# Kernel tuning notes

Measured on AMD Instinct MI355X. Metric: run time of the kernel, lower is better.

Reference implementation:

```python
import jax, jax.numpy as jnp
import numpy as np

H = 3  # hidden size (matches nn.LSTM(3, 3, ...))


def _lstm_dir(x, Wih, Whh, bih, bhh, reverse):
    """One direction of one LSTM layer. x: [B,T,D]; PyTorch gate order i,f,g,o."""
    B = x.shape[0]
    xT = jnp.swapaxes(x, 0, 1)  # [T,B,D]
    # Precompute input projection for all timesteps (memory-bound GEMM once).
    x_proj = jnp.einsum('tbd,gd->tbg', xT, Wih) + (bih + bhh)  # [T,B,4H]

    def step(carry, xp):
        h, c = carry
        gates = xp + h @ Whh.T  # [B,4H]
        i = jax.nn.sigmoid(gates[:, :H])
        f = jax.nn.sigmoid(gates[:, H:2 * H])
        g = jnp.tanh(gates[:, 2 * H:3 * H])
        o = jax.nn.sigmoid(gates[:, 3 * H:])
        c = f * c + i * g
        h = o * jnp.tanh(c)
        return (h, c), h

    init = (jnp.zeros((B, H), x.dtype), jnp.zeros((B, H), x.dtype))
    _, hs = jax.lax.scan(step, init, x_proj, reverse=reverse)
    return jnp.swapaxes(hs, 0, 1)  # [B,T,H], time-aligned with input


def setup_inputs() -> dict:
    key = jax.random.key(0)
    ks = jax.random.split(key, 20)
    B, T = 8192, 512
    k = 1.0 / np.sqrt(H)

    def u(kk, shape):
        return jax.random.uniform(kk, shape, jnp.float32, -k, k)

    inp = {"x": jax.random.normal(ks[0], (B, T, 3), jnp.float32)}
    # layer 0: input dim 3; layer 1: input dim 2*H = 6
    inp.update({
        "W_ih_l0": u(ks[1], (4 * H, 3)),  "W_hh_l0": u(ks[2], (4 * H, H)),
        "b_ih_l0": u(ks[3], (4 * H,)),    "b_hh_l0": u(ks[4], (4 * H,)),
        "W_ih_l0r": u(ks[5], (4 * H, 3)), "W_hh_l0r": u(ks[6], (4 * H, H)),
        "b_ih_l0r": u(ks[7], (4 * H,)),   "b_hh_l0r": u(ks[8], (4 * H,)),
        "W_ih_l1": u(ks[9], (4 * H, 2 * H)),  "W_hh_l1": u(ks[10], (4 * H, H)),
        "b_ih_l1": u(ks[11], (4 * H,)),       "b_hh_l1": u(ks[12], (4 * H,)),
        "W_ih_l1r": u(ks[13], (4 * H, 2 * H)),"W_hh_l1r": u(ks[14], (4 * H, H)),
        "b_ih_l1r": u(ks[15], (4 * H,)),      "b_hh_l1r": u(ks[16], (4 * H,)),
        "W_lin": u(ks[17], (1, 2 * H)),       "b_lin": u(ks[18], (1,)),
    })
    return inp


def reference(x, W_ih_l0, W_hh_l0, b_ih_l0, b_hh_l0,
              W_ih_l0r, W_hh_l0r, b_ih_l0r, b_hh_l0r,
              W_ih_l1, W_hh_l1, b_ih_l1, b_hh_l1,
              W_ih_l1r, W_hh_l1r, b_ih_l1r, b_hh_l1r,
              W_lin, b_lin):
    # layer 0 (bidirectional)
    y0 = jnp.concatenate([
        _lstm_dir(x, W_ih_l0, W_hh_l0, b_ih_l0, b_hh_l0, False),
        _lstm_dir(x, W_ih_l0r, W_hh_l0r, b_ih_l0r, b_hh_l0r, True),
    ], axis=-1)  # [B,T,6]
    # layer 1 (bidirectional)
    y1 = jnp.concatenate([
        _lstm_dir(y0, W_ih_l1, W_hh_l1, b_ih_l1, b_hh_l1, False),
        _lstm_dir(y0, W_ih_l1r, W_hh_l1r, b_ih_l1r, b_hh_l1r, True),
    ], axis=-1)  # [B,T,6]
    last = y1[:, -1, :]  # [B,6]  (output sequence at final timestep)
    out = last @ W_lin.T + b_lin  # [B,1]
    return jax.nn.sigmoid(out.reshape(-1))  # [B]
```

## Files before the change

kernel.cpp:

```cpp
#include <hip/hip_runtime.h>


#define B_ 8192
#define T_ 512
#define LOG2E 1.4426950408889634f

typedef float v2f __attribute__((ext_vector_type(2)));

__device__ __forceinline__ float rcp_(float x)  { return __builtin_amdgcn_rcpf(x); }
__device__ __forceinline__ float exp2_(float x) { return __builtin_amdgcn_exp2f(x); }
__device__ __forceinline__ float sigm_(float x) {
  return rcp_(1.0f + exp2_(-LOG2E * x));
}
__device__ __forceinline__ float tanh_(float x) {
  return 1.0f - 2.0f * rcp_(1.0f + exp2_(2.0f * LOG2E * x));
}
__device__ __forceinline__ float act_(float p) { return rcp_(1.f + exp2_(p)); }

__device__ __forceinline__ v2f sp(float s) { return (v2f){s, s}; }
__device__ __forceinline__ v2f pkfma(v2f a, float b, v2f c) {
  return __builtin_elementwise_fma(a, sp(b), c);
}

template <int CTRL>
__device__ __forceinline__ float dppf(float v) {
  int s = __float_as_int(v);
  return __int_as_float(__builtin_amdgcn_update_dpp(s, s, CTRL, 0xF, 0xF, false));
}
#define QP0 0x00
#define QP1 0x55
#define QP2 0xAA
#define SHL4 0x104
#define SHR4 0x114

#define CELL_TAIL(HOUT)                                                   \
    float r0v = act_(pv.x);                                               \
    float ayv = act_(pv.y);             \
    float axv = __builtin_fmaf(avx, r0v, dvx);  \
    float slx = dppf<SHL4>(axv), sly = dppf<SHL4>(ayv);                   \
    float srx = dppf<SHR4>(axv), sry = dppf<SHR4>(ayv);                   \
    float pig = axv * (qgo ? srx : slx);           \
    float gf  = qgo ? sry : ayv;                                          \
    float gO  = qgo ? ayv : sly;                                          \
    c = __builtin_fmaf(gf, c, pig);                                       \
    float th = __builtin_fmaf(                                            \
        2.f, rcp_(1.f + exp2_(-2.f * LOG2E * c)), -1.f);                  \
    h = gO * th;                                                          \
    ha0 = dppf<QP0>(h); ha1 = dppf<QP1>(h); ha2 = dppf<QP2>(h);           \
    HOUT = h;

__global__ __launch_bounds__(256, 2) void lstm_l0_both(
    const float* __restrict__ x,
    const float* __restrict__ Wf_ih, const float* __restrict__ Wf_hh,
    const float* __restrict__ bf_ih, const float* __restrict__ bf_hh,
    const float* __restrict__ Wr_ih, const float* __restrict__ Wr_hh,
    const float* __restrict__ br_ih, const float* __restrict__ br_hh,
    float* __restrict__ y0f,
    float* __restrict__ y0b)
{
  int tid  = blockIdx.x * 256 + threadIdx.x;
  int b    = tid >> 4;
  int lane = tid & 15;
  bool dirb = lane >= 8;
  bool qgo  = (lane & 4) != 0;
  int j = lane & 3; int jj = (j < 3) ? j : 0;
  const int ra = (qgo ? 6 : 0) + jj, rb = ra + 3;
  const float kx = qgo ? (-2.f * LOG2E) : (-LOG2E);
  const float ky = -LOG2E;
  const float avx = qgo ? 2.f : 1.f;
  const float dvx = qgo ? -1.f : 0.f;

  const float* Wi = dirb ? Wr_ih : Wf_ih;
  const float* Wh = dirb ? Wr_hh : Wf_hh;
  const float* bi = dirb ? br_ih : bf_ih;
  const float* bh = dirb ? br_hh : bf_hh;

  v2f w0 = {Wi[ra*3+0]*kx, Wi[rb*3+0]*ky},
      w1 = {Wi[ra*3+1]*kx, Wi[rb*3+1]*ky},
      w2 = {Wi[ra*3+2]*kx, Wi[rb*3+2]*ky};
  v2f u0 = {Wh[ra*3+0]*kx, Wh[rb*3+0]*ky},
      u1 = {Wh[ra*3+1]*kx, Wh[rb*3+1]*ky},
      u2 = {Wh[ra*3+2]*kx, Wh[rb*3+2]*ky};
  v2f b2 = {(bi[ra]+bh[ra])*kx, (bi[rb]+bh[rb])*ky};

  float h = 0.f, c = 0.f, ha0 = 0.f, ha1 = 0.f, ha2 = 0.f;

  const float4* xq = (const float4*)(x + (size_t)b * (T_ * 3));
  int offA  = dirb ? 63 * 6 : 0;
  int offB  = offA + (dirb ? -6 : 6);
  int dstep = dirb ? -12 : 12;
  float* ywp = (dirb ? y0b : y0f) + (size_t)b * (T_ * 3) + jj * 8
             + (dirb ? 63 * 24 : 0);
  int ystep = dirb ? -24 : 24;

  float hs0, hs1, hs2, hs3, hs4, hs5, hs6, hs7;
  float4 p0, p1, p2, p3, p4, p5, q0, q1, q2, q3, q4, q5;

#define LDA(off, r0_, r1_, r2_, r3_, r4_, r5_) do {                       \
    const float4* _p = xq + (off);                                        \
    r0_ = _p[0]; r1_ = _p[1]; r2_ = _p[2];                                \
    r3_ = _p[3]; r4_ = _p[4]; r5_ = _p[5];                                \
    __builtin_amdgcn_sched_barrier(0); } while (0)

#define STEPA(xf0, xf1, xf2, xb0, xb1, xb2, HOUT) do {                    \
    float x0 = dirb ? (xb0) : (xf0);                                      \
    float x1 = dirb ? (xb1) : (xf1);                                      \
    float x2 = dirb ? (xb2) : (xf2);                                      \
    v2f pv = pkfma(w0, x0, b2); pv = pkfma(w1, x1, pv);                   \
    pv = pkfma(w2, x2, pv);                                               \
    v2f uv = u0 * sp(ha0); uv = pkfma(u1, ha1, uv);                       \
    uv = pkfma(u2, ha2, uv);                                              \
    pv = pv + uv;                                                         \
    CELL_TAIL(HOUT) } while (0)

#define PROCA(r0_, r1_, r2_, r3_, r4_, r5_) do {                          \
    STEPA(r0_.x, r0_.y, r0_.z,  r5_.y, r5_.z, r5_.w, hs0);                \
    STEPA(r0_.w, r1_.x, r1_.y,  r4_.z, r4_.w, r5_.x, hs1);                \
    STEPA(r1_.z, r1_.w, r2_.x,  r3_.w, r4_.x, r4_.y, hs2);                \
    STEPA(r2_.y, r2_.z, r2_.w,  r3_.x, r3_.y, r3_.z, hs3);                \
    STEPA(r3_.x, r3_.y, r3_.z,  r2_.y, r2_.z, r2_.w, hs4);                \
    STEPA(r3_.w, r4_.x, r4_.y,  r1_.z, r1_.w, r2_.x, hs5);                \
    STEPA(r4_.z, r4_.w, r5_.x,  r0_.w, r1_.x, r1_.y, hs6);                \
    STEPA(r5_.y, r5_.z, r5_.w,  r0_.x, r0_.y, r0_.z, hs7); } while (0)

#define FLUSHA() do {                                                     \
    float sv0 = dirb ? hs7 : hs0, sv1 = dirb ? hs6 : hs1;                 \
    float sv2 = dirb ? hs5 : hs2, sv3 = dirb ? hs4 : hs3;                 \
    float sv4 = dirb ? hs3 : hs4, sv5 = dirb ? hs2 : hs5;                 \
    float sv6 = dirb ? hs1 : hs6, sv7 = dirb ? hs0 : hs7;                 \
    if ((lane & 7) < 3) {                                                 \
      float4* _o = (float4*)ywp;                                          \
      _o[0] = make_float4(sv0, sv1, sv2, sv3);                            \
      _o[1] = make_float4(sv4, sv5, sv6, sv7);                            \
    }                                                                     \
    ywp += ystep; } while (0)

  LDA(offA, p0, p1, p2, p3, p4, p5); offA += dstep;
  LDA(offB, q0, q1, q2, q3, q4, q5); offB += dstep;
  for (int it = 0; it < 32; ++it) {
    PROCA(p0, p1, p2, p3, p4, p5);
    FLUSHA();
    if (it < 31) { LDA(offA, p0, p1, p2, p3, p4, p5); offA += dstep; }
    PROCA(q0, q1, q2, q3, q4, q5);
    FLUSHA();
    if (it < 31) { LDA(offB, q0, q1, q2, q3, q4, q5); offB += dstep; }
  }
#undef LDA
#undef STEPA
#undef PROCA
#undef FLUSHA
}

__global__ __launch_bounds__(256, 1) void lstm_l1_fwd(
    const float* __restrict__ Wih1, const float* __restrict__ Whh1,
    const float* __restrict__ bih1, const float* __restrict__ bhh1,
    const float* __restrict__ Wih1r,
    const float* __restrict__ bih1r, const float* __restrict__ bhh1r,
    const float* __restrict__ Wlin, const float* __restrict__ blin,
    const float* __restrict__ y0f,
    const float* __restrict__ y0b,
    float* __restrict__ out)
{
  int tid  = blockIdx.x * 256 + threadIdx.x;
  int b    = tid >> 3;
  int lane = tid & 7;
  bool qgo = (lane & 4) != 0;
  int j = lane & 3; int jj = (j < 3) ? j : 0;
  const int ra = (qgo ? 6 : 0) + jj, rb = ra + 3;
  const float kx = qgo ? (-2.f * LOG2E) : (-LOG2E);
  const float ky = -LOG2E;
  const float avx = qgo ? 2.f : 1.f;
  const float dvx = qgo ? -1.f : 0.f;

  v2f w0 = {Wih1[ra*6+0]*kx, Wih1[rb*6+0]*ky},
      w1 = {Wih1[ra*6+1]*kx, Wih1[rb*6+1]*ky},
      w2 = {Wih1[ra*6+2]*kx, Wih1[rb*6+2]*ky},
      w3 = {Wih1[ra*6+3]*kx, Wih1[rb*6+3]*ky},
      w4 = {Wih1[ra*6+4]*kx, Wih1[rb*6+4]*ky},
      w5 = {Wih1[ra*6+5]*kx, Wih1[rb*6+5]*ky};
  v2f u0 = {Whh1[ra*3+0]*kx, Whh1[rb*3+0]*ky},
      u1 = {Whh1[ra*3+1]*kx, Whh1[rb*3+1]*ky},
      u2 = {Whh1[ra*3+2]*kx, Whh1[rb*3+2]*ky};
  v2f b2 = {(bih1[ra]+bhh1[ra])*kx, (bih1[rb]+bhh1[rb])*ky};

  const float4* yfq = (const float4*)(y0f + (size_t)b * (T_ * 3));
  const float4* ybq = (const float4*)(y0b + (size_t)b * (T_ * 3));

  const float* ufp = y0f + (size_t)b * (T_ * 3) + 63 * 24 + 7;
  const float* ubp = y0b + (size_t)b * (T_ * 3) + 63 * 24 + 7;
  float uf0 = ufp[0], uf1 = ufp[8], uf2 = ufp[16];
  float ub0 = ubp[0], ub1 = ubp[8], ub2 = ubp[16];

  float h = 0.f, c = 0.f, ha0 = 0.f, ha1 = 0.f, ha2 = 0.f;
  float hs0, hs1, hs2, hs3, hs4, hs5, hs6, hs7;
  float4 pf0, pf1, pf2, pf3, pf4, pf5, pb0, pb1, pb2, pb3, pb4, pb5;
  float4 qf0, qf1, qf2, qf3, qf4, qf5, qb0, qb1, qb2, qb3, qb4, qb5;

#define LDB(blk, F0,F1,F2,F3,F4,F5, G0,G1,G2,G3,G4,G5) do {               \
    const float4* _f = yfq + (blk) * 6;                                   \
    const float4* _g = ybq + (blk) * 6;                                   \
    F0 = _f[0]; F1 = _f[1]; F2 = _f[2];                                   \
    F3 = _f[3]; F4 = _f[4]; F5 = _f[5];                                   \
    G0 = _g[0]; G1 = _g[1]; G2 = _g[2];                                   \
    G3 = _g[3]; G4 = _g[4]; G5 = _g[5];                                   \
    __builtin_amdgcn_sched_barrier(0); } while (0)

#define STEPB(f0, f1, f2, g0, g1, g2, HOUT) do {                          \
    v2f pv = pkfma(w0, (f0), b2); pv = pkfma(w1, (f1), pv);               \
    pv = pkfma(w2, (f2), pv);                                             \
    v2f nv = w3 * sp(g0); nv = pkfma(w4, (g1), nv);                       \
    nv = pkfma(w5, (g2), nv);                                             \
    v2f uv = u0 * sp(ha0); uv = pkfma(u1, ha1, uv);                       \
    uv = pkfma(u2, ha2, uv);                                              \
    pv = (pv + nv) + uv;                                                  \
    CELL_TAIL(HOUT) } while (0)

#define PROCB(F0,F1,F2,F3,F4,F5, G0,G1,G2,G3,G4,G5) do {                  \
    STEPB(F0.x, F2.x, F4.x,  G0.x, G2.x, G4.x, hs0);                      \
    STEPB(F0.y, F2.y, F4.y,  G0.y, G2.y, G4.y, hs1);                      \
    STEPB(F0.z, F2.z, F4.z,  G0.z, G2.z, G4.z, hs2);                      \
    STEPB(F0.w, F2.w, F4.w,  G0.w, G2.w, G4.w, hs3);                      \
    STEPB(F1.x, F3.x, F5.x,  G1.x, G3.x, G5.x, hs4);                      \
    STEPB(F1.y, F3.y, F5.y,  G1.y, G3.y, G5.y, hs5);                      \
    STEPB(F1.z, F3.z, F5.z,  G1.z, G3.z, G5.z, hs6);                      \
    STEPB(F1.w, F3.w, F5.w,  G1.w, G3.w, G5.w, hs7); } while (0)

  LDB(0, pf0,pf1,pf2,pf3,pf4,pf5, pb0,pb1,pb2,pb3,pb4,pb5);
  LDB(1, qf0,qf1,qf2,qf3,qf4,qf5, qb0,qb1,qb2,qb3,qb4,qb5);
  for (int it = 0; it < 32; ++it) {
    PROCB(pf0,pf1,pf2,pf3,pf4,pf5, pb0,pb1,pb2,pb3,pb4,pb5);
    if (it < 31) LDB(2*it+2, pf0,pf1,pf2,pf3,pf4,pf5, pb0,pb1,pb2,pb3,pb4,pb5);
    PROCB(qf0,qf1,qf2,qf3,qf4,qf5, qb0,qb1,qb2,qb3,qb4,qb5);
    if (it < 31) LDB(2*it+3, qf0,qf1,qf2,qf3,qf4,qf5, qb0,qb1,qb2,qb3,qb4,qb5);
  }
  (void)hs0; (void)hs1; (void)hs2; (void)hs3;
  (void)hs4; (void)hs5; (void)hs6; (void)hs7;

  float h1b;
  {
    v2f r0 = {Wih1r[ra*6+0]*kx, Wih1r[rb*6+0]*ky},
        r1 = {Wih1r[ra*6+1]*kx, Wih1r[rb*6+1]*ky},
        r2 = {Wih1r[ra*6+2]*kx, Wih1r[rb*6+2]*ky},
        r3 = {Wih1r[ra*6+3]*kx, Wih1r[rb*6+3]*ky},
        r4 = {Wih1r[ra*6+4]*kx, Wih1r[rb*6+4]*ky},
        r5 = {Wih1r[ra*6+5]*kx, Wih1r[rb*6+5]*ky};
    v2f br = {(bih1r[ra]+bhh1r[ra])*kx, (bih1r[rb]+bhh1r[rb])*ky};
    v2f qv = pkfma(r0, uf0, br); qv = pkfma(r1, uf1, qv);
    qv = pkfma(r2, uf2, qv);     qv = pkfma(r3, ub0, qv);
    qv = pkfma(r4, ub1, qv);     qv = pkfma(r5, ub2, qv);
    float r0v = act_(qv.x);
    float ayv = act_(qv.y);
    float axv = __builtin_fmaf(avx, r0v, dvx);
    float slx = dppf<SHL4>(axv), sly = dppf<SHL4>(ayv);
    float srx = dppf<SHR4>(axv);
    float gi = qgo ? srx : axv;
    float gG = qgo ? axv : slx;
    float gO = qgo ? ayv : sly;
    float cb = gi * gG;
    h1b = gO * tanh_(cb);
  }

  float part = 0.f;
  if (!qgo && j < 3) part = __builtin_fmaf(Wlin[j], h, Wlin[3 + j] * h1b);
  part += __shfl_xor(part, 1, 8);
  part += __shfl_xor(part, 2, 8);
  part += __shfl_xor(part, 4, 8);
  if (lane == 0) out[b] = sigm_(part + blin[0]);
#undef LDB
#undef STEPB
#undef PROCB
}

extern "C" void kernel_launch(void* const* d_in, const int* in_sizes, int n_in,
                              void* d_out, int out_size, void* d_ws, size_t ws_size,
                              hipStream_t stream) {
  const float* x        = (const float*)d_in[0];
  const float* W_ih_l0  = (const float*)d_in[1];
  const float* W_hh_l0  = (const float*)d_in[2];
  const float* b_ih_l0  = (const float*)d_in[3];
  const float* b_hh_l0  = (const float*)d_in[4];
  const float* W_ih_l0r = (const float*)d_in[5];
  const float* W_hh_l0r = (const float*)d_in[6];
  const float* b_ih_l0r = (const float*)d_in[7];
  const float* b_hh_l0r = (const float*)d_in[8];
  const float* W_ih_l1  = (const float*)d_in[9];
  const float* W_hh_l1  = (const float*)d_in[10];
  const float* b_ih_l1  = (const float*)d_in[11];
  const float* b_hh_l1  = (const float*)d_in[12];
  const float* W_ih_l1r = (const float*)d_in[13];
  const float* b_ih_l1r = (const float*)d_in[15];
  const float* b_hh_l1r = (const float*)d_in[16];
  const float* W_lin    = (const float*)d_in[17];
  const float* b_lin    = (const float*)d_in[18];

  float* y0f = (float*)d_ws;
  float* y0b = (float*)d_ws + (size_t)B_ * T_ * 3;
  float* out = (float*)d_out;

  lstm_l0_both<<<(B_ * 16) / 256, 256, 0, stream>>>(
      x, W_ih_l0, W_hh_l0, b_ih_l0, b_hh_l0,
      W_ih_l0r, W_hh_l0r, b_ih_l0r, b_hh_l0r, y0f, y0b);

  lstm_l1_fwd<<<(B_ * 8) / 256, 256, 0, stream>>>(
      W_ih_l1, W_hh_l1, b_ih_l1, b_hh_l1,
      W_ih_l1r, b_ih_l1r, b_hh_l1r,
      W_lin, b_lin, y0f, y0b, out);
}
```

Measured before the change: 172.8 us.

## Remap layer-0 LSTM to four lanes per direction computing all gates per lane

Layer 0 used 16 lanes per batch row, with each lane computing two gate pre-activations and exchanging them through DPP shifts. Now 4 lanes per row and direction each compute all four gates for one hidden unit, with forward and backward directions split into separate thread ranges and specialised by a template. Input loads are spread across the quad and broadcast with quad-permute DPP. This halves the thread count and removes the gate-exchange shuffles, but raises per-thread arithmetic and register use.

```diff
diff --git a/kernel.cpp b/kernel.cpp
--- a/kernel.cpp
+++ b/kernel.cpp
@@ -27,129 +27,172 @@
   int s = __float_as_int(v);
   return __int_as_float(__builtin_amdgcn_update_dpp(s, s, CTRL, 0xF, 0xF, false));
 }
-#define QP0 0x00
-#define QP1 0x55
-#define QP2 0xAA
+#define QP0 dppf<0x00>
+#define QP1 dppf<0x55>
+#define QP2 dppf<0xAA>
+#define QP3 dppf<0xFF>
 #define SHL4 0x104
 #define SHR4 0x114
 
+
+template <bool DIRB>
+__device__ __forceinline__ void l0_run(
+    const float* __restrict__ x,
+    const float* __restrict__ Wi, const float* __restrict__ Wh,
+    const float* __restrict__ bi, const float* __restrict__ bh,
+    float* __restrict__ yout, int b, int jl)
+{
+  const int jj = (jl < 3) ? jl : 0;
+  const int ri = jj, rf = 3 + jj, rg = 6 + jj, ro = 9 + jj;
+  const float sL = -LOG2E, sG = -2.f * LOG2E;
+
+  float wi_i0 = Wi[ri*3+0]*sL, wi_i1 = Wi[ri*3+1]*sL, wi_i2 = Wi[ri*3+2]*sL;
+  float wi_f0 = Wi[rf*3+0]*sL, wi_f1 = Wi[rf*3+1]*sL, wi_f2 = Wi[rf*3+2]*sL;
+  float wi_g0 = Wi[rg*3+0]*sG, wi_g1 = Wi[rg*3+1]*sG, wi_g2 = Wi[rg*3+2]*sG;
+  float wi_o0 = Wi[ro*3+0]*sL, wi_o1 = Wi[ro*3+1]*sL, wi_o2 = Wi[ro*3+2]*sL;
+  float wh_i0 = Wh[ri*3+0]*sL, wh_i1 = Wh[ri*3+1]*sL, wh_i2 = Wh[ri*3+2]*sL;
+  float wh_f0 = Wh[rf*3+0]*sL, wh_f1 = Wh[rf*3+1]*sL, wh_f2 = Wh[rf*3+2]*sL;
+  float wh_g0 = Wh[rg*3+0]*sG, wh_g1 = Wh[rg*3+1]*sG, wh_g2 = Wh[rg*3+2]*sG;
+  float wh_o0 = Wh[ro*3+0]*sL, wh_o1 = Wh[ro*3+1]*sL, wh_o2 = Wh[ro*3+2]*sL;
+  float b_i = (bi[ri]+bh[ri])*sL, b_f = (bi[rf]+bh[rf])*sL;
+  float b_g = (bi[rg]+bh[rg])*sG, b_o = (bi[ro]+bh[ro])*sL;
+
+  float h = 0.f, c = 0.f, ha0 = 0.f, ha1 = 0.f, ha2 = 0.f;
+  float hs0, hs1, hs2, hs3, hs4, hs5, hs6, hs7;
+
+  const float*  xrow = x + (size_t)b * (T_ * 3);
+  const float4* xq4  = (const float4*)xrow;
+  const float2* xq2  = (const float2*)(xrow);
+  float* ybase = yout + (size_t)b * (T_ * 3) + jj * 8;
+
+  float4 pA; float2 pB; float4 qA; float2 qB;
+
+#define LDQ(blk, A_, B_) do {                                             \
+    A_ = xq4[(blk) * 6 + jl];                                             \
+    B_ = xq2[(blk) * 12 + 8 + jl];                                        \
+    __builtin_amdgcn_sched_barrier(0); } while (0)
+
+#define STEPS(X0, X1, X2, HOUT) do {                                      \
+    float _x0 = (X0), _x1 = (X1), _x2 = (X2);                             \
+    float _pi = __builtin_fmaf(wi_i0, _x0, b_i);                          \
+    _pi = __builtin_fmaf(wi_i1, _x1, _pi);                                \
+    _pi = __builtin_fmaf(wi_i2, _x2, _pi);                                \
+    float _qi = wh_i0 * ha0;                                              \
+    _qi = __builtin_fmaf(wh_i1, ha1, _qi);                                \
+    _qi = __builtin_fmaf(wh_i2, ha2, _qi);                                \
+    float _pf = __builtin_fmaf(wi_f0, _x0, b_f);                          \
+    _pf = __builtin_fmaf(wi_f1, _x1, _pf);                                \
+    _pf = __builtin_fmaf(wi_f2, _x2, _pf);                                \
+    float _qf = wh_f0 * ha0;                                              \
+    _qf = __builtin_fmaf(wh_f1, ha1, _qf);                                \
+    _qf = __builtin_fmaf(wh_f2, ha2, _qf);                                \
+    float _pg = __builtin_fmaf(wi_g0, _x0, b_g);                          \
+    _pg = __builtin_fmaf(wi_g1, _x1, _pg);                                \
+    _pg = __builtin_fmaf(wi_g2, _x2, _pg);                                \
+    float _qg = wh_g0 * ha0;                                              \
+    _qg = __builtin_fmaf(wh_g1, ha1, _qg);                                \
+    _qg = __builtin_fmaf(wh_g2, ha2, _qg);                                \
+    float _po = __builtin_fmaf(wi_o0, _x0, b_o);                          \
+    _po = __builtin_fmaf(wi_o1, _x1, _po);                                \
+    _po = __builtin_fmaf(wi_o2, _x2, _po);                                \
+    float _qo = wh_o0 * ha0;                                              \
+    _qo = __builtin_fmaf(wh_o1, ha1, _qo);                                \
+    _qo = __builtin_fmaf(wh_o2, ha2, _qo);                                \
+    float _ig = act_(_pi + _qi);                                          \
+    float _fg = act_(_pf + _qf);                                          \
+    float _gg = __builtin_fmaf(2.f, act_(_pg + _qg), -1.f);               \
+    float _og = act_(_po + _qo);                                          \
+    c = __builtin_fmaf(_fg, c, _ig * _gg);                                \
+    float _th = __builtin_fmaf(                                           \
+        2.f, rcp_(1.f + exp2_(-2.f * LOG2E * c)), -1.f);                  \
+    h = _og * _th;                                                        \
+    ha0 = QP0(h); ha1 = QP1(h); ha2 = QP2(h);                             \
+    HOUT = h; } while (0)
+
+#define S0(A_, B_) STEPS(QP0(A_.x), QP0(A_.y), QP0(A_.z), hs0)
+#define S1(A_, B_) STEPS(QP0(A_.w), QP1(A_.x), QP1(A_.y), hs1)
+#define S2(A_, B_) STEPS(QP1(A_.z), QP1(A_.w), QP2(A_.x), hs2)
+#define S3(A_, B_) STEPS(QP2(A_.y), QP2(A_.z), QP2(A_.w), hs3)
+#define S4(A_, B_) STEPS(QP3(A_.x), QP3(A_.y), QP3(A_.z), hs4)
+#define S5(A_, B_) STEPS(QP3(A_.w), QP0(B_.x), QP0(B_.y), hs5)
+#define S6(A_, B_) STEPS(QP1(B_.x), QP1(B_.y), QP2(B_.x), hs6)
+#define S7(A_, B_) STEPS(QP2(B_.y), QP3(B_.x), QP3(B_.y), hs7)
+
+#define PROCQ(A_, B_) do {                                                \
+    if (DIRB) { S7(A_,B_); S6(A_,B_); S5(A_,B_); S4(A_,B_);               \
+                S3(A_,B_); S2(A_,B_); S1(A_,B_); S0(A_,B_); }             \
+    else      { S0(A_,B_); S1(A_,B_); S2(A_,B_); S3(A_,B_);               \
+                S4(A_,B_); S5(A_,B_); S6(A_,B_); S7(A_,B_); } } while (0)
+
+#define STQ(blk) do {                                                     \
+    if (jl < 3) {                                                         \
+      float4* _o = (float4*)(ybase + (blk) * 24);                         \
+      _o[0] = make_float4(hs0, hs1, hs2, hs3);                            \
+      _o[1] = make_float4(hs4, hs5, hs6, hs7);                            \
+    } } while (0)
+
+#define BLK(k) (DIRB ? (63 - (k)) : (k))
+
+  LDQ(BLK(0), pA, pB);
+  LDQ(BLK(1), qA, qB);
+  for (int k = 0; k < 64; k += 2) {
+    PROCQ(pA, pB);
+    STQ(BLK(k));
+    if (k + 2 < 64) LDQ(BLK(k + 2), pA, pB);
+    PROCQ(qA, qB);
+    STQ(BLK(k + 1));
+    if (k + 3 < 64) LDQ(BLK(k + 3), qA, qB);
+  }
+#undef LDQ
+#undef STEPS
+#undef S0
+#undef S1
+#undef S2
+#undef S3
+#undef S4
+#undef S5
+#undef S6
+#undef S7
+#undef PROCQ
+#undef STQ
+#undef BLK
+}
+
+__global__ __launch_bounds__(256, 2) void lstm_l0_scalar(
+    const float* __restrict__ x,
+    const float* __restrict__ Wf_ih, const float* __restrict__ Wf_hh,
+    const float* __restrict__ bf_ih, const float* __restrict__ bf_hh,
+    const float* __restrict__ Wr_ih, const float* __restrict__ Wr_hh,
+    const float* __restrict__ br_ih, const float* __restrict__ br_hh,
+    float* __restrict__ y0f, float* __restrict__ y0b)
+{
+  int gid = blockIdx.x * 256 + threadIdx.x;
+  const int nfwd = B_ * 4;
+  if (gid < nfwd) {
+    int b = gid >> 2, jl = gid & 3;
+    l0_run<false>(x, Wf_ih, Wf_hh, bf_ih, bf_hh, y0f, b, jl);
+  } else {
+    int g2 = gid - nfwd;
+    int b = g2 >> 2, jl = g2 & 3;
+    l0_run<true>(x, Wr_ih, Wr_hh, br_ih, br_hh, y0b, b, jl);
+  }
+}
+
 #define CELL_TAIL(HOUT)                                                   \
     float r0v = act_(pv.x);                                               \
-    float ayv = act_(pv.y);             \
-    float axv = __builtin_fmaf(avx, r0v, dvx);  \
+    float ayv = act_(pv.y);                                               \
+    float axv = __builtin_fmaf(avx, r0v, dvx);                            \
     float slx = dppf<SHL4>(axv), sly = dppf<SHL4>(ayv);                   \
     float srx = dppf<SHR4>(axv), sry = dppf<SHR4>(ayv);                   \
-    float pig = axv * (qgo ? srx : slx);           \
+    float pig = axv * (qgo ? srx : slx);                                  \
     float gf  = qgo ? sry : ayv;                                          \
     float gO  = qgo ? ayv : sly;                                          \
     c = __builtin_fmaf(gf, c, pig);                                       \
     float th = __builtin_fmaf(                                            \
         2.f, rcp_(1.f + exp2_(-2.f * LOG2E * c)), -1.f);                  \
     h = gO * th;                                                          \
-    ha0 = dppf<QP0>(h); ha1 = dppf<QP1>(h); ha2 = dppf<QP2>(h);           \
+    ha0 = QP0(h); ha1 = QP1(h); ha2 = QP2(h);                             \
     HOUT = h;
-
-__global__ __launch_bounds__(256, 2) void lstm_l0_both(
-    const float* __restrict__ x,
-    const float* __restrict__ Wf_ih, const float* __restrict__ Wf_hh,
-    const float* __restrict__ bf_ih, const float* __restrict__ bf_hh,
-    const float* __restrict__ Wr_ih, const float* __restrict__ Wr_hh,
-    const float* __restrict__ br_ih, const float* __restrict__ br_hh,
-    float* __restrict__ y0f,
-    float* __restrict__ y0b)
-{
-  int tid  = blockIdx.x * 256 + threadIdx.x;
-  int b    = tid >> 4;
-  int lane = tid & 15;
-  bool dirb = lane >= 8;
-  bool qgo  = (lane & 4) != 0;
-  int j = lane & 3; int jj = (j < 3) ? j : 0;
-  const int ra = (qgo ? 6 : 0) + jj, rb = ra + 3;
-  const float kx = qgo ? (-2.f * LOG2E) : (-LOG2E);
-  const float ky = -LOG2E;
-  const float avx = qgo ? 2.f : 1.f;
-  const float dvx = qgo ? -1.f : 0.f;
-
-  const float* Wi = dirb ? Wr_ih : Wf_ih;
-  const float* Wh = dirb ? Wr_hh : Wf_hh;
-  const float* bi = dirb ? br_ih : bf_ih;
-  const float* bh = dirb ? br_hh : bf_hh;
-
-  v2f w0 = {Wi[ra*3+0]*kx, Wi[rb*3+0]*ky},
-      w1 = {Wi[ra*3+1]*kx, Wi[rb*3+1]*ky},
-      w2 = {Wi[ra*3+2]*kx, Wi[rb*3+2]*ky};
-  v2f u0 = {Wh[ra*3+0]*kx, Wh[rb*3+0]*ky},
-      u1 = {Wh[ra*3+1]*kx, Wh[rb*3+1]*ky},
-      u2 = {Wh[ra*3+2]*kx, Wh[rb*3+2]*ky};
-  v2f b2 = {(bi[ra]+bh[ra])*kx, (bi[rb]+bh[rb])*ky};
-
-  float h = 0.f, c = 0.f, ha0 = 0.f, ha1 = 0.f, ha2 = 0.f;
-
-  const float4* xq = (const float4*)(x + (size_t)b * (T_ * 3));
-  int offA  = dirb ? 63 * 6 : 0;
-  int offB  = offA + (dirb ? -6 : 6);
-  int dstep = dirb ? -12 : 12;
-  float* ywp = (dirb ? y0b : y0f) + (size_t)b * (T_ * 3) + jj * 8
-             + (dirb ? 63 * 24 : 0);
-  int ystep = dirb ? -24 : 24;
-
-  float hs0, hs1, hs2, hs3, hs4, hs5, hs6, hs7;
-  float4 p0, p1, p2, p3, p4, p5, q0, q1, q2, q3, q4, q5;
-
-#define LDA(off, r0_, r1_, r2_, r3_, r4_, r5_) do {                       \
-    const float4* _p = xq + (off);                                        \
-    r0_ = _p[0]; r1_ = _p[1]; r2_ = _p[2];                                \
-    r3_ = _p[3]; r4_ = _p[4]; r5_ = _p[5];                                \
-    __builtin_amdgcn_sched_barrier(0); } while (0)
-
-#define STEPA(xf0, xf1, xf2, xb0, xb1, xb2, HOUT) do {                    \
-    float x0 = dirb ? (xb0) : (xf0);                                      \
-    float x1 = dirb ? (xb1) : (xf1);                                      \
-    float x2 = dirb ? (xb2) : (xf2);                                      \
-    v2f pv = pkfma(w0, x0, b2); pv = pkfma(w1, x1, pv);                   \
-    pv = pkfma(w2, x2, pv);                                               \
-    v2f uv = u0 * sp(ha0); uv = pkfma(u1, ha1, uv);                       \
-    uv = pkfma(u2, ha2, uv);                                              \
-    pv = pv + uv;                                                         \
-    CELL_TAIL(HOUT) } while (0)
-
-#define PROCA(r0_, r1_, r2_, r3_, r4_, r5_) do {                          \
-    STEPA(r0_.x, r0_.y, r0_.z,  r5_.y, r5_.z, r5_.w, hs0);                \
-    STEPA(r0_.w, r1_.x, r1_.y,  r4_.z, r4_.w, r5_.x, hs1);                \
-    STEPA(r1_.z, r1_.w, r2_.x,  r3_.w, r4_.x, r4_.y, hs2);                \
-    STEPA(r2_.y, r2_.z, r2_.w,  r3_.x, r3_.y, r3_.z, hs3);                \
-    STEPA(r3_.x, r3_.y, r3_.z,  r2_.y, r2_.z, r2_.w, hs4);                \
-    STEPA(r3_.w, r4_.x, r4_.y,  r1_.z, r1_.w, r2_.x, hs5);                \
-    STEPA(r4_.z, r4_.w, r5_.x,  r0_.w, r1_.x, r1_.y, hs6);                \
-    STEPA(r5_.y, r5_.z, r5_.w,  r0_.x, r0_.y, r0_.z, hs7); } while (0)
-
-#define FLUSHA() do {                                                     \
-    float sv0 = dirb ? hs7 : hs0, sv1 = dirb ? hs6 : hs1;                 \
-    float sv2 = dirb ? hs5 : hs2, sv3 = dirb ? hs4 : hs3;                 \
-    float sv4 = dirb ? hs3 : hs4, sv5 = dirb ? hs2 : hs5;                 \
-    float sv6 = dirb ? hs1 : hs6, sv7 = dirb ? hs0 : hs7;                 \
-    if ((lane & 7) < 3) {                                                 \
-      float4* _o = (float4*)ywp;                                          \
-      _o[0] = make_float4(sv0, sv1, sv2, sv3);                            \
-      _o[1] = make_float4(sv4, sv5, sv6, sv7);                            \
-    }                                                                     \
-    ywp += ystep; } while (0)
-
-  LDA(offA, p0, p1, p2, p3, p4, p5); offA += dstep;
-  LDA(offB, q0, q1, q2, q3, q4, q5); offB += dstep;
-  for (int it = 0; it < 32; ++it) {
-    PROCA(p0, p1, p2, p3, p4, p5);
-    FLUSHA();
-    if (it < 31) { LDA(offA, p0, p1, p2, p3, p4, p5); offA += dstep; }
-    PROCA(q0, q1, q2, q3, q4, q5);
-    FLUSHA();
-    if (it < 31) { LDA(offB, q0, q1, q2, q3, q4, q5); offB += dstep; }
-  }
-#undef LDA
-#undef STEPA
-#undef PROCA
-#undef FLUSHA
-}
 
 __global__ __launch_bounds__(256, 1) void lstm_l1_fwd(
     const float* __restrict__ Wih1, const float* __restrict__ Whh1,
@@ -157,8 +200,7 @@
     const float* __restrict__ Wih1r,
     const float* __restrict__ bih1r, const float* __restrict__ bhh1r,
     const float* __restrict__ Wlin, const float* __restrict__ blin,
-    const float* __restrict__ y0f,
-    const float* __restrict__ y0b,
+    const float* __restrict__ y0f, const float* __restrict__ y0b,
     float* __restrict__ out)
 {
   int tid  = blockIdx.x * 256 + threadIdx.x;
@@ -297,7 +339,7 @@
   float* y0b = (float*)d_ws + (size_t)B_ * T_ * 3;
   float* out = (float*)d_out;
 
-  lstm_l0_both<<<(B_ * 16) / 256, 256, 0, stream>>>(
+  lstm_l0_scalar<<<(B_ * 4 * 2) / 256, 256, 0, stream>>>(
       x, W_ih_l0, W_hh_l0, b_ih_l0, b_hh_l0,
       W_ih_l0r, W_hh_l0r, b_ih_l0r, b_hh_l0r, y0f, y0b);
 
```

After: 151.9 us. -12.1%, faster.
